# Kernel tuning notes

Measured on AMD Instinct MI355X. Metric: run time of the kernel, lower is better.

Reference implementation:

```python
import jax, jax.numpy as jnp
import numpy as np

B, L, C, S, W, R = 2, 16, 64, 64, 128, 32
MOD_HIDDEN = 32


def _conv3d(x, k, b, pad_hw):
    # x: (B,C,L,S,W), k: (O,I,1,kh,kw)
    y = jax.lax.conv_general_dilated(
        x, k, window_strides=(1, 1, 1),
        padding=((0, 0), (pad_hw, pad_hw), (pad_hw, pad_hw)),
        dimension_numbers=('NCDHW', 'OIDHW', 'NCDHW'))
    return y + b[None, :, None, None, None]


def setup_inputs() -> dict:
    key = jax.random.key(0)
    ks = jax.random.split(key, 16)
    d = {}
    d['x'] = jax.random.normal(ks[0], (B, L, C, S, W), jnp.float32)
    u1 = jax.random.uniform(ks[1], (C, R), jnp.float32)
    u2 = jax.random.uniform(ks[2], (C, R), jnp.float32)
    r_min, r_max = 0.8, 0.99
    d['nu_log'] = jnp.log(-0.5 * jnp.log(u1 * (r_max ** 2 - r_min ** 2) + r_min ** 2))
    d['theta_log'] = jnp.log(u2 * jnp.float32(2 * np.pi))
    d['disp_nu'] = jnp.zeros((C, R), jnp.float32)
    d['disp_theta'] = jnp.zeros((C, R), jnp.float32)
    d['mlp_w1'] = jax.random.normal(ks[3], (C, MOD_HIDDEN), jnp.float32) / np.sqrt(C).astype(np.float32)
    d['mlp_b1'] = jnp.zeros((MOD_HIDDEN,), jnp.float32)
    d['mlp_w2'] = jax.random.normal(ks[4], (MOD_HIDDEN, C * R * 2), jnp.float32) / np.sqrt(MOD_HIDDEN).astype(np.float32)
    d['mlp_b2'] = jnp.zeros((C * R * 2,), jnp.float32)
    d['forcing_scale'] = jnp.float32(0.1)
    d['U_row_r'] = jax.random.normal(ks[5], (C, S, R), jnp.float32) / np.sqrt(S).astype(np.float32)
    d['U_row_i'] = jax.random.normal(ks[6], (C, S, R), jnp.float32) / np.sqrt(S).astype(np.float32)
    d['V_col_r'] = jax.random.normal(ks[7], (C, W, R), jnp.float32) / np.sqrt(W).astype(np.float32)
    d['V_col_i'] = jax.random.normal(ks[8], (C, W, R), jnp.float32) / np.sqrt(W).astype(np.float32)
    d['proj_W_r'] = jax.random.normal(ks[9], (C, C), jnp.float32) / np.sqrt(C).astype(np.float32)
    d['proj_W_i'] = jax.random.normal(ks[10], (C, C), jnp.float32) / np.sqrt(C).astype(np.float32)
    d['proj_b_r'] = jnp.zeros((C,), jnp.float32)
    d['proj_b_i'] = jnp.zeros((C,), jnp.float32)
    fan = np.sqrt(C * 9).astype(np.float32)
    d['convr_k'] = jax.random.normal(ks[11], (C, C, 1, 3, 3), jnp.float32) / fan
    d['convr_b'] = jnp.zeros((C,), jnp.float32)
    d['convi_k'] = jax.random.normal(ks[12], (C, C, 1, 3, 3), jnp.float32) / fan
    d['convi_b'] = jnp.zeros((C,), jnp.float32)
    d['fuse_k'] = jax.random.normal(ks[13], (C, 2 * C, 1, 1, 1), jnp.float32) / np.sqrt(2 * C).astype(np.float32)
    d['fuse_b'] = jnp.zeros((C,), jnp.float32)
    d['ln_g'] = jnp.ones((S, W), jnp.float32)
    d['ln_b'] = jnp.zeros((S, W), jnp.float32)
    return d


def reference(x, nu_log, theta_log, disp_nu, disp_theta, mlp_w1, mlp_b1,
              mlp_w2, mlp_b2, forcing_scale, U_row_r, U_row_i, V_col_r,
              V_col_i, proj_W_r, proj_W_i, proj_b_r, proj_b_i, convr_k,
              convr_b, convi_k, convi_b, fuse_k, fuse_b, ln_g, ln_b):
    # Diagonal LRU poles lam = exp(-exp(nu) + i*exp(theta)), per (C,R)
    nu = jnp.exp(nu_log + disp_nu)
    theta = jnp.exp(theta_log + disp_theta)
    lam = jnp.exp(jax.lax.complex(-nu, theta))
    gamma = jnp.sqrt(jnp.clip(1.0 - jnp.abs(lam) ** 2, 1e-6, None))

    # Selective input-dependent forcing from spatially-pooled context
    ctx = x.mean(axis=(-2, -1))  # (B,L,C)
    f = jnp.tanh(ctx @ mlp_w1 + mlp_b1) @ mlp_w2 + mlp_b2
    f = f.reshape(ctx.shape[0], ctx.shape[1], C, R, 2)
    forcing = forcing_scale * jax.lax.complex(f[..., 0], f[..., 1])  # (B,L,C,R)

    # Low-rank complex spatial projection to rank-R state per channel
    U = jax.lax.complex(U_row_r, U_row_i)  # (C,S,R)
    V = jax.lax.complex(V_col_r, V_col_i)  # (C,W,R)
    xc = x.astype(jnp.complex64)
    u = jnp.einsum('blcsw,csr->blcwr', xc, jnp.conj(U))
    u = jnp.einsum('blcwr,cwr->blcr', u, jnp.conj(V))  # (B,L,C,R)
    u = gamma * u * (1.0 + forcing)

    # Diagonal linear recurrence h_t = lam*h_{t-1} + u_t via associative scan over L
    A = jnp.broadcast_to(lam[None, None], u.shape)

    def comb(e1, e2):
        a1, b1 = e1
        a2, b2 = e2
        return a1 * a2, a2 * b1 + b2

    _, h = jax.lax.associative_scan(comb, (A, u), axis=1)

    # Reconstruct spatial field from low-rank states
    t = jnp.einsum('blcr,csr->blcsr', h, U)
    y = jnp.einsum('blcsr,cwr->blcsw', t, V)  # (B,L,C,S,W) complex

    projW = jax.lax.complex(proj_W_r, proj_W_i)
    projb = jax.lax.complex(proj_b_r, proj_b_i)
    y = jnp.einsum('blcsw,oc->blosw', y, projW) + projb[None, None, :, None, None]

    # Post-recurrence spatial convs on real/imag parts, fuse, layernorm, residual
    yr = jnp.transpose(jnp.real(y), (0, 2, 1, 3, 4))  # (B,C,L,S,W)
    yi = jnp.transpose(jnp.imag(y), (0, 2, 1, 3, 4))
    yr = _conv3d(yr, convr_k, convr_b, 1)
    yi = _conv3d(yi, convi_k, convi_b, 1)
    fused = _conv3d(jnp.concatenate([yr, yi], axis=1), fuse_k, fuse_b, 0)
    fused = jnp.transpose(fused, (0, 2, 1, 3, 4))  # (B,L,C,S,W)

    mu = fused.mean(axis=(-2, -1), keepdims=True)
    var = fused.var(axis=(-2, -1), keepdims=True)
    normed = (fused - mu) / jnp.sqrt(var + 1e-5) * ln_g + ln_b
    return normed + x
```

## Files before the change

kernel.cpp:

```cpp
#include <hip/hip_runtime.h>

typedef unsigned short u16;
typedef unsigned int u32;
typedef __attribute__((ext_vector_type(8))) short short8;
typedef __attribute__((ext_vector_type(4))) float f32x4;
typedef __attribute__((ext_vector_type(16))) float f32x16;

constexpr int B = 2, L = 16, C = 64, S = 64, W = 128, R = 32, MH = 32;
constexpr int BL = B * L;
constexpr int SW = S * W;
constexpr int CR = C * R;
constexpr int F2 = C * R * 2;
constexpr int NVE = 64 * 4 * 4 * 64 * 8;
constexpr int NVD = 64 * 8 * 2 * 64 * 8;

constexpr int NB_PREP  = 8;
constexpr int NB_KEFF  = 289;
constexpr int NB_APACK = 64;
constexpr int NB_VPACK = (NVE + 2 * NVD + 255) / 256;
constexpr int NB_ALL   = NB_PREP + NB_KEFF + NB_APACK + NB_VPACK;

__device__ __forceinline__ float us2f(u16 h) { return __uint_as_float(((u32)h) << 16); }
__device__ __forceinline__ float bf_lo(u32 u) { return __uint_as_float(u << 16); }
__device__ __forceinline__ float bf_hi(u32 u) { return __uint_as_float(u & 0xffff0000u); }
__device__ __forceinline__ u16 f2bu(float f) {
  u32 u = __float_as_uint(f);
  u32 r = (u + 0x7fffu + ((u >> 16) & 1u)) >> 16;
  return (u16)r;
}
__device__ __forceinline__ u32 pack2(float lo, float hi) {
  return (u32)f2bu(lo) | ((u32)f2bu(hi) << 16);
}

__global__ void k_prep_all(
    const float* __restrict__ nu_log, const float* __restrict__ th_log,
    const float* __restrict__ dnu, const float* __restrict__ dth,
    float* __restrict__ lamr, float* __restrict__ lami, float* __restrict__ gam,
    const float* __restrict__ fuse_k, const float* __restrict__ fuse_b,
    const float* __restrict__ convr_k, const float* __restrict__ convr_b,
    const float* __restrict__ convi_k, const float* __restrict__ convi_b,
    u16* __restrict__ keff_bf, float* __restrict__ biaseff,
    const float* __restrict__ pWr, const float* __restrict__ pWi,
    u16* __restrict__ aproj,
    const float* __restrict__ Vr, const float* __restrict__ Vi,
    u16* __restrict__ venc, u16* __restrict__ vdecr, u16* __restrict__ vdeci) {
  int bid = blockIdx.x;
  int t = threadIdx.x;
  if (bid < NB_PREP) {
    int i = bid * 256 + t;
    if (i >= CR) return;
    float nu = expf(nu_log[i] + dnu[i]);
    float th = expf(th_log[i] + dth[i]);
    float mag = expf(-nu);
    lamr[i] = mag * cosf(th);
    lami[i] = mag * sinf(th);
    gam[i] = sqrtf(fmaxf(1.0f - mag * mag, 1e-6f));
  } else if (bid < NB_PREP + NB_KEFF) {
    int i = (bid - NB_PREP) * 256 + t;
    if (i < C * 2 * C * 9) {
      int o = i / (2 * C * 9);
      int rem = i - o * (2 * C * 9);
      int cin2 = rem / 9;
      int seg = rem - cin2 * 9;
      const float* ck = (cin2 < C) ? convr_k : convi_k;
      int cin = cin2 & (C - 1);
      int fbase = o * 2 * C + ((cin2 < C) ? 0 : C);
      float acc = 0.f;
      for (int m = 0; m < C; ++m)
        acc += fuse_k[fbase + m] * ck[(m * C + cin) * 9 + seg];
      int kslice = cin2 >> 4;
      int kk = cin2 & 15;
      int lane = (o & 31) | ((kk >> 3) << 5);
      int j = kk & 7;
      int m_tile = o >> 5;
      keff_bf[((((seg * 8 + kslice) * 2 + m_tile) * 64 + lane) << 3) + j] = f2bu(acc);
    } else if (i < C * 2 * C * 9 + C) {
      int o = i - C * 2 * C * 9;
      float acc = fuse_b[o];
      for (int m = 0; m < C; ++m) {
        acc += fuse_k[o * 2 * C + m] * convr_b[m];
        acc += fuse_k[o * 2 * C + C + m] * convi_b[m];
      }
      biaseff[o] = acc;
    }
  } else if (bid < NB_PREP + NB_KEFF + NB_APACK) {
    int i = (bid - NB_PREP - NB_KEFF) * 256 + t;
    if (i >= 128 * 128) return;
    int m = i >> 7, k = i & 127;
    int c = k >> 1, im = k & 1;
    int o = m & 63;
    float v;
    if (m < 64) v = im ? -pWi[o * 64 + c] : pWr[o * 64 + c];
    else        v = im ?  pWr[o * 64 + c] : pWi[o * 64 + c];
    aproj[i] = f2bu(v);
  } else {
    int i = (bid - NB_PREP - NB_KEFF - NB_APACK) * 256 + t;
    if (i < NVE) {
      int j = i & 7, lane = (i >> 3) & 63, ks = (i >> 9) & 3;
      int wv = (i >> 11) & 3, c = i >> 13;
      int n = wv * 16 + (lane & 15);
      int w = ks * 32 + ((lane >> 4) & 3) * 8 + j;
      float v = (n < 32) ? Vr[(size_t)c * 4096 + w * 32 + n]
                         : -Vi[(size_t)c * 4096 + w * 32 + (n - 32)];
      venc[i] = f2bu(v);
    } else if (i < NVE + 2 * NVD) {
      int ii = i - NVE;
      int isI = 0;
      if (ii >= NVD) { ii -= NVD; isI = 1; }
      int j = ii & 7, lane = (ii >> 3) & 63, ks = (ii >> 9) & 1;
      int g = (ii >> 10) & 7, c = ii >> 13;
      int w = g * 16 + (lane & 15);
      int k = ks * 32 + ((lane >> 4) & 3) * 8 + j;
      float v;
      if (!isI) v = (k < 32) ? Vr[(size_t)c * 4096 + w * 32 + k]
                             : -Vi[(size_t)c * 4096 + w * 32 + (k - 32)];
      else      v = (k < 32) ? Vi[(size_t)c * 4096 + w * 32 + k]
                             :  Vr[(size_t)c * 4096 + w * 32 + (k - 32)];
      (isI ? vdeci : vdecr)[ii] = f2bu(v);
    }
  }
}

__global__ __launch_bounds__(256) void k_mlp(
    const float* __restrict__ ctx, const float* __restrict__ w1, const float* __restrict__ b1,
    const float* __restrict__ w2, const float* __restrict__ b2, const float* __restrict__ fscale,
    float* __restrict__ forcing) {
  int bl = blockIdx.x >> 4;
  int kt = blockIdx.x & 15;
  int k0 = kt * 256;
  __shared__ float cv[C];
  __shared__ float hid[MH];
  __shared__ float lw2[MH * 256];
  int t = threadIdx.x;
  if (t < C) cv[t] = ctx[bl * C + t];
  for (int i = t; i < MH * 64; i += 256) {
    int j = i >> 6, q = i & 63;
    ((float4*)lw2)[i] = ((const float4*)(w2 + (size_t)j * F2 + k0))[q];
  }
  __syncthreads();
  if (t < MH) {
    float a = b1[t];
    for (int c2 = 0; c2 < C; ++c2) a += cv[c2] * w1[c2 * MH + t];
    hid[t] = tanhf(a);
  }
  __syncthreads();
  float scale = fscale[0];
  float a = b2[k0 + t];
#pragma unroll
  for (int j = 0; j < MH; ++j) a += hid[j] * lw2[j * 256 + t];
  forcing[(size_t)bl * F2 + k0 + t] = scale * a;
}

__global__ __launch_bounds__(256) void k_enc(
    const float* __restrict__ x, const u16* __restrict__ venc,
    const float* __restrict__ Ur, const float* __restrict__ Ui,
    float* __restrict__ ctx, float* __restrict__ u) {
  int blc = blockIdx.x;
  int c = blc & (C - 1);
  __shared__ __align__(16) char smem[35968];
  u16* xt = (u16*)smem;
  float* uldr = (float*)(smem + 17408);
  float* uldi = uldr + 2048;
  float* y1  = (float*)smem;
  float* part = (float*)(smem + 33792);
  float* red = (float*)(smem + 35840);
  int t = threadIdx.x;
  int lane = t & 63, wv = t >> 6;
  short8 bf[4];
  {
    const short8* vep = (const short8*)venc + ((size_t)(c * 4 + wv) * 4) * 64 + lane;
#pragma unroll
    for (int ks = 0; ks < 4; ++ks) bf[ks] = vep[ks * 64];
  }
  float sm = 0.f;
  {
    const float4* xp = (const float4*)(x + (size_t)blc * SW);
    for (int i = t; i < SW / 4; i += 256) {
      float4 v = xp[i];
      sm += v.x + v.y + v.z + v.w;
      int idx = i * 4, s = idx >> 7, w = idx & 127;
      u32* d = (u32*)&xt[s * 136 + w];
      d[0] = pack2(v.x, v.y);
      d[1] = pack2(v.z, v.w);
    }
  }
#pragma unroll
  for (int o = 32; o > 0; o >>= 1) sm += __shfl_down(sm, o, 64);
  if (lane == 0) red[wv] = sm;
  {
    const float4* urp = (const float4*)(Ur + (size_t)c * 2048);
    const float4* uip = (const float4*)(Ui + (size_t)c * 2048);
    float4* dr = (float4*)uldr;
    float4* di = (float4*)uldi;
    for (int i = t; i < 512; i += 256) { dr[i] = urp[i]; di[i] = uip[i]; }
  }
  __syncthreads();
  if (t == 0) ctx[blc] = (red[0] + red[1] + red[2] + red[3]) * (1.f / SW);
  int quad = lane >> 4, l15 = lane & 15;
  f32x4 zf = {0.f, 0.f, 0.f, 0.f};
  f32x4 acc[4] = {zf, zf, zf, zf};
#pragma unroll
  for (int ks = 0; ks < 4; ++ks) {
    int kofs = ks * 32 + quad * 8;
#pragma unroll
    for (int mt = 0; mt < 4; ++mt) {
      short8 af = *(const short8*)&xt[(mt * 16 + l15) * 136 + kofs];
      acc[mt] = __builtin_amdgcn_mfma_f32_16x16x32_bf16(af, bf[ks], acc[mt], 0, 0, 0);
    }
  }
  __syncthreads();
#pragma unroll
  for (int mt = 0; mt < 4; ++mt)
#pragma unroll
    for (int reg = 0; reg < 4; ++reg)
      y1[(mt * 16 + quad * 4 + reg) * 65 + wv * 16 + l15] = acc[mt][reg];
  __syncthreads();
  {
    int r = t & 31, sg = t >> 5;
    float pr = 0.f, pi = 0.f;
#pragma unroll
    for (int k = 0; k < 8; ++k) {
      int s = sg * 8 + k;
      float yr = y1[s * 65 + r], yi = y1[s * 65 + 32 + r];
      float ur = uldr[s * 32 + r], ui = uldi[s * 32 + r];
      pr += ur * yr + ui * yi;
      pi += ur * yi - ui * yr;
    }
    part[sg * 64 + r * 2]     = pr;
    part[sg * 64 + r * 2 + 1] = pi;
  }
  __syncthreads();
  if (t < 32) {
    float pr = 0.f, pi = 0.f;
#pragma unroll
    for (int sg = 0; sg < 8; ++sg) {
      pr += part[sg * 64 + t * 2];
      pi += part[sg * 64 + t * 2 + 1];
    }
    u[((size_t)blc * R + t) * 2]     = pr;
    u[((size_t)blc * R + t) * 2 + 1] = pi;
  }
}

__global__ __launch_bounds__(256) void k_scan(
    const float* __restrict__ lamr, const float* __restrict__ lami,
    const float* __restrict__ gam, const float* __restrict__ forcing,
    const float* __restrict__ u, float* __restrict__ h) {
  int b = blockIdx.x >> 4;
  int c0 = (blockIdx.x & 15) * 128;
  __shared__ float uld[L][256];
  __shared__ float fld[L][256];
  int t = threadIdx.x;
#pragma unroll
  for (int l = 0; l < L; ++l) {
    size_t base = ((size_t)(b * L + l) * CR + c0) * 2;
    uld[l][t] = u[base + t];
    fld[l][t] = forcing[base + t];
  }
  __syncthreads();
  if (t < 128) {
    int cr = c0 + t;
    float lr = lamr[cr], li = lami[cr], g = gam[cr];
    float hr = 0.f, hi = 0.f;
#pragma unroll
    for (int l = 0; l < L; ++l) {
      float ur0 = uld[l][t * 2], ui0 = uld[l][t * 2 + 1];
      float fr = fld[l][t * 2], fi = fld[l][t * 2 + 1];
      float ofr = 1.f + fr;
      float ur = g * (ur0 * ofr - ui0 * fi);
      float ui = g * (ur0 * fi + ui0 * ofr);
      float nr = lr * hr - li * hi + ur;
      float ni = lr * hi + li * hr + ui;
      hr = nr; hi = ni;
      uld[l][t * 2] = hr; uld[l][t * 2 + 1] = hi;
    }
  }
  __syncthreads();
#pragma unroll
  for (int l = 0; l < L; ++l) {
    size_t base = ((size_t)(b * L + l) * CR + c0) * 2;
    h[base + t] = uld[l][t];
  }
}

__global__ __launch_bounds__(256) void k_decode(
    const float* __restrict__ h,
    const float* __restrict__ Ur, const float* __restrict__ Ui,
    const u16* __restrict__ vdecr, const u16* __restrict__ vdeci,
    u32* __restrict__ y_cm32, int bl_base) {
  int bid = blockIdx.x;
  int c = bid & 63;
  int blh = bid >> 6;
  int bl = bl_base + blh;
  __shared__ __align__(16) u16 ldA[64 * 72];
  int t = threadIdx.x;
  {
    const float* hp = h + ((size_t)(bl * C + c) * R) * 2;
    const float* urp = Ur + (size_t)c * (S * R);
    const float* uip = Ui + (size_t)c * (S * R);
    for (int p = t; p < S * R; p += 256) {
      int s = p >> 5, r = p & 31;
      float hr = hp[r * 2], hi = hp[r * 2 + 1];
      float ur = urp[p], ui = uip[p];
      ldA[s * 72 + r]      = f2bu(hr * ur - hi * ui);
      ldA[s * 72 + 32 + r] = f2bu(hr * ui + hi * ur);
    }
  }
  __syncthreads();
  int lane = t & 63, q = t >> 6;
  int quad = lane >> 4, l15 = lane & 15;
  const short8* vdr = (const short8*)vdecr + (size_t)c * 16 * 64;
  const short8* vdi = (const short8*)vdeci + (size_t)c * 16 * 64;
  f32x4 zf = {0.f, 0.f, 0.f, 0.f};
  f32x4 accr[4][2], acci[4][2];
#pragma unroll
  for (int mt = 0; mt < 4; ++mt)
#pragma unroll
    for (int nt = 0; nt < 2; ++nt) { accr[mt][nt] = zf; acci[mt][nt] = zf; }
#pragma unroll
  for (int ks = 0; ks < 2; ++ks) {
    int kofs = ks * 32 + quad * 8;
    short8 af[4];
#pragma unroll
    for (int mt = 0; mt < 4; ++mt)
      af[mt] = *(const short8*)&ldA[(mt * 16 + l15) * 72 + kofs];
#pragma unroll
    for (int nt = 0; nt < 2; ++nt) {
      int g = q * 2 + nt;
      short8 br = vdr[(g * 2 + ks) * 64 + lane];
      short8 bi = vdi[(g * 2 + ks) * 64 + lane];
#pragma unroll
      for (int mt = 0; mt < 4; ++mt) {
        accr[mt][nt] = __builtin_amdgcn_mfma_f32_16x16x32_bf16(af[mt], br, accr[mt][nt], 0, 0, 0);
        acci[mt][nt] = __builtin_amdgcn_mfma_f32_16x16x32_bf16(af[mt], bi, acci[mt][nt], 0, 0, 0);
      }
    }
  }
  u32* dst = y_cm32 + ((size_t)(blh * 64 + c) << 13);
#pragma unroll
  for (int mt = 0; mt < 4; ++mt) {
#pragma unroll
    for (int nt = 0; nt < 2; ++nt) {
      int w = q * 32 + nt * 16 + l15;
#pragma unroll
      for (int reg = 0; reg < 4; ++reg) {
        int s = mt * 16 + quad * 4 + reg;
        dst[s * 128 + w] = pack2(accr[mt][nt][reg], acci[mt][nt][reg]);
      }
    }
  }
}

__global__ __launch_bounds__(256) void k_proj(
    const u32* __restrict__ y_cm32, const u16* __restrict__ aproj,
    const float* __restrict__ pbr, const float* __restrict__ pbi,
    u16* __restrict__ ynhwc, int bl_base) {
  int bid = blockIdx.x;
  int ntile = bid & 15;
  int blh = bid >> 4;
  int bl = bl_base + blh;
  __shared__ __align__(16) u16 lda[128 * 136];
  __shared__ __align__(16) u32 ldb[128 * 68];
  __shared__ float ldbias[128];
  int t = threadIdx.x;
  for (int i = t; i < 128 * 16; i += 256) {
    int m = i >> 4, qq = i & 15;
    ((uint4*)&lda[m * 136])[qq] = ((const uint4*)&aproj[m * 128])[qq];
  }
  if (t < 128) ldbias[t] = t < 64 ? pbr[t] : pbi[t - 64];

  int lane = t & 63, wv = t >> 6;
  int quad = lane >> 4, l15 = lane & 15;
  int cidx = t & 63, seg = t >> 6;
  f32x4 zf = {0.f, 0.f, 0.f, 0.f};

  for (int chunk = 0; chunk < 4; ++chunk) {
    int n0 = ntile * 512 + chunk * 128;
    __syncthreads();
    {
      const uint4* src = (const uint4*)(y_cm32 + (((size_t)(blh * 64 + cidx)) << 13) + n0 + seg * 32);
      u32 tmp[32];
#pragma unroll
      for (int qq = 0; qq < 8; ++qq) {
        uint4 v = src[qq];
        tmp[qq * 4] = v.x; tmp[qq * 4 + 1] = v.y; tmp[qq * 4 + 2] = v.z; tmp[qq * 4 + 3] = v.w;
      }
#pragma unroll
      for (int j = 0; j < 32; ++j)
        ldb[(seg * 32 + j) * 68 + cidx] = tmp[j];
    }
    __syncthreads();
    f32x4 acc[8][2];
#pragma unroll
    for (int mt = 0; mt < 8; ++mt) { acc[mt][0] = zf; acc[mt][1] = zf; }
    const u16* ldb16 = (const u16*)ldb;
#pragma unroll
    for (int ks = 0; ks < 4; ++ks) {
      int kofs = ks * 32 + quad * 8;
      short8 af[8];
#pragma unroll
      for (int mt = 0; mt < 8; ++mt)
        af[mt] = *(const short8*)&lda[(mt * 16 + l15) * 136 + kofs];
#pragma unroll
      for (int nt = 0; nt < 2; ++nt) {
        int nrow = wv * 32 + nt * 16 + l15;
        short8 bf = *(const short8*)&ldb16[nrow * 136 + kofs];
#pragma unroll
        for (int mt = 0; mt < 8; ++mt)
          acc[mt][nt] = __builtin_amdgcn_mfma_f32_16x16x32_bf16(af[mt], bf, acc[mt][nt], 0, 0, 0);
      }
    }
#pragma unroll
    for (int nt = 0; nt < 2; ++nt) {
      int n = n0 + wv * 32 + nt * 16 + l15;
      u16* drow = ynhwc + (((size_t)bl * SW + n) << 7);
#pragma unroll
      for (int mt = 0; mt < 8; ++mt) {
        int ch = mt * 16 + quad * 4;
        u32 lo = pack2(acc[mt][nt][0] + ldbias[ch],     acc[mt][nt][1] + ldbias[ch + 1]);
        u32 hi = pack2(acc[mt][nt][2] + ldbias[ch + 2], acc[mt][nt][3] + ldbias[ch + 3]);
        u32* dp = (u32*)(drow + ch);
        dp[0] = lo; dp[1] = hi;
      }
    }
  }
}

__global__ __launch_bounds__(256, 4) void k_conv(
    const u16* __restrict__ ynhwc, const u16* __restrict__ keff_bf,
    const float* __restrict__ biaseff, u16* __restrict__ fused) {
  int bid = blockIdx.x;
  int wt = bid & 1;
  int st = (bid >> 1) & 31;
  int bl = bid >> 6;
  int s0 = st * 2;
  int w0 = wt * 64;
  __shared__ __align__(16) u16 win[4][66][72];
  int t = threadIdx.x;
  int c_lo = (wt == 0) ? 1 : 0;
  int c_hi = (wt == 0) ? 66 : 65;
  uint4 z4 = make_uint4(0u, 0u, 0u, 0u);

  int lane = t & 63;
  int wv = t >> 6;
  int sr = wv & 1;
  int mt = wv >> 1;
  int l31 = lane & 31, khalf = lane >> 5;

  f32x16 acc0, acc1;
#pragma unroll
  for (int i = 0; i < 16; ++i) { acc0[i] = 0.f; acc1[i] = 0.f; }
  const short8* ap = (const short8*)keff_bf;
  short8 abuf[2];

#pragma unroll
  for (int p = 0; p < 2; ++p) {
    if (p) __syncthreads();
    for (int rr = 0; rr < 4; ++rr) {
      int rs = s0 - 1 + rr;
      if (rs < 0 || rs >= S) {
        for (int i = t; i < 66 * 8; i += 256) {
          int col = i >> 3, q = i & 7;
          ((uint4*)&win[rr][col][0])[q] = z4;
        }
      } else {
        if (wt == 0 && t < 8) ((uint4*)&win[rr][0][0])[t] = z4;
        if (wt == 1 && t < 8) ((uint4*)&win[rr][65][0])[t] = z4;
        const uint4* src = (const uint4*)(ynhwc +
            (((size_t)bl * S + rs) * W + (w0 - 1 + c_lo)) * 128 + p * 64);
        int n4 = (c_hi - c_lo) * 8;
        for (int i = t; i < n4; i += 256) {
          int col = i >> 3, q = i & 7;
          ((uint4*)&win[rr][c_lo + col][0])[q] = src[col * 16 + q];
        }
      }
    }
    __syncthreads();

    abuf[0] = ap[((p * 4) * 2 + mt) * 64 + lane];

#pragma unroll
    for (int m = 0; m < 36; ++m) {
      const int cur = m & 1;
      const int nxt = cur ^ 1;
      if (m < 35) {
        const int m1 = m + 1;
        abuf[nxt] = ap[((((m1 >> 2) * 8 + p * 4 + (m1 & 3)) * 2 + mt)) * 64 + lane];
      }
      const int seg = m >> 2;
      const int k4 = m & 3;
      const int dr = seg / 3;
      const int dc = seg - dr * 3;
      const u16* bb = &win[sr + dr][l31 + dc][k4 * 16 + khalf * 8];
      short8 b0 = *(const short8*)bb;
      short8 b1 = *(const short8*)(bb + 32 * 72);
      acc0 = __builtin_amdgcn_mfma_f32_32x32x16_bf16(abuf[cur], b0, acc0, 0, 0, 0);
      acc1 = __builtin_amdgcn_mfma_f32_32x32x16_bf16(abuf[cur], b1, acc1, 0, 0, 0);
    }
  }

  int s_out = s0 + sr;
#pragma unroll
  for (int reg = 0; reg < 16; ++reg) {
    int o = mt * 32 + (reg & 3) + 8 * (reg >> 2) + 4 * khalf;
    float bias = biaseff[o];
    size_t rowoff = ((size_t)(bl * C + o) * S + s_out) * W;
    fused[rowoff + w0 + l31]      = f2bu(acc0[reg] + bias);
    fused[rowoff + w0 + 32 + l31] = f2bu(acc1[reg] + bias);
  }
}

__global__ __launch_bounds__(256) void k_ln(
    const u16* __restrict__ fused,
    const float* __restrict__ ln_g, const float* __restrict__ ln_b,
    const float* __restrict__ x, float* __restrict__ out) {
  int blc = blockIdx.x;
  __shared__ u16 fs[SW];
  __shared__ float red[12];
  int t = threadIdx.x;
  const uint4* fp = (const uint4*)(fused + (size_t)blc * SW);
  float sm = 0.f, sq = 0.f;
  for (int i = t; i < SW / 8; i += 256) {
    uint4 v = fp[i];
    ((uint4*)fs)[i] = v;
    float f0 = bf_lo(v.x), f1 = bf_hi(v.x), f2 = bf_lo(v.y), f3 = bf_hi(v.y);
    float f4 = bf_lo(v.z), f5 = bf_hi(v.z), f6 = bf_lo(v.w), f7 = bf_hi(v.w);
    sm += f0 + f1 + f2 + f3 + f4 + f5 + f6 + f7;
    sq += f0 * f0 + f1 * f1 + f2 * f2 + f3 * f3 + f4 * f4 + f5 * f5 + f6 * f6 + f7 * f7;
  }
#pragma unroll
  for (int off = 32; off > 0; off >>= 1) {
    sm += __shfl_down(sm, off, 64);
    sq += __shfl_down(sq, off, 64);
  }
  int lane = t & 63, wid = t >> 6;
  if (lane == 0) { red[wid * 2] = sm; red[wid * 2 + 1] = sq; }
  __syncthreads();
  if (t == 0) {
    float S1 = red[0] + red[2] + red[4] + red[6];
    float S2 = red[1] + red[3] + red[5] + red[7];
    float mu = S1 * (1.f / SW);
    float var = S2 * (1.f / SW) - mu * mu;
    red[8] = mu;
    red[9] = rsqrtf(var + 1e-5f);
  }
  __syncthreads();
  float mu = red[8], rstd = red[9];
  const float4* xp4 = (const float4*)(x + (size_t)blc * SW);
  float4* op4 = (float4*)(out + (size_t)blc * SW);
  const float4* g4 = (const float4*)ln_g;
  const float4* b4 = (const float4*)ln_b;
  const uint2* fs2 = (const uint2*)fs;
  for (int i = t; i < SW / 4; i += 256) {
    uint2 fv = fs2[i];
    float4 xv = xp4[i];
    float4 gv = g4[i];
    float4 bv = b4[i];
    float4 o;
    o.x = (bf_lo(fv.x) - mu) * rstd * gv.x + bv.x + xv.x;
    o.y = (bf_hi(fv.x) - mu) * rstd * gv.y + bv.y + xv.y;
    o.z = (bf_lo(fv.y) - mu) * rstd * gv.z + bv.z + xv.z;
    o.w = (bf_hi(fv.y) - mu) * rstd * gv.w + bv.w + xv.w;
    op4[i] = o;
  }
}

extern "C" void kernel_launch(void* const* d_in, const int* in_sizes, int n_in,
                              void* d_out, int out_size, void* d_ws, size_t ws_size,
                              hipStream_t stream) {
  (void)in_sizes; (void)n_in; (void)out_size; (void)ws_size;
  const float* x       = (const float*)d_in[0];
  const float* nu_log  = (const float*)d_in[1];
  const float* th_log  = (const float*)d_in[2];
  const float* dnu     = (const float*)d_in[3];
  const float* dth     = (const float*)d_in[4];
  const float* w1      = (const float*)d_in[5];
  const float* b1      = (const float*)d_in[6];
  const float* w2      = (const float*)d_in[7];
  const float* b2      = (const float*)d_in[8];
  const float* fscale  = (const float*)d_in[9];
  const float* Ur      = (const float*)d_in[10];
  const float* Ui      = (const float*)d_in[11];
  const float* Vr      = (const float*)d_in[12];
  const float* Vi      = (const float*)d_in[13];
  const float* pWr     = (const float*)d_in[14];
  const float* pWi     = (const float*)d_in[15];
  const float* pbr     = (const float*)d_in[16];
  const float* pbi     = (const float*)d_in[17];
  const float* convr_k = (const float*)d_in[18];
  const float* convr_b = (const float*)d_in[19];
  const float* convi_k = (const float*)d_in[20];
  const float* convi_b = (const float*)d_in[21];
  const float* fuse_k  = (const float*)d_in[22];
  const float* fuse_b  = (const float*)d_in[23];
  const float* ln_g    = (const float*)d_in[24];
  const float* ln_b    = (const float*)d_in[25];
  float* out = (float*)d_out;

  char* ws = (char*)d_ws;
  float* lamr    = (float*)ws;
  float* lami    = lamr + 2048;
  float* gam     = lami + 2048;
  float* biaseff = gam + 2048;
  float* ctx     = biaseff + 64;
  float* forcing = ctx + 2048;
  float* ubuf    = forcing + 131072;
  float* hbuf    = ubuf + 131072;
  u16* keff_bf   = (u16*)(hbuf + 131072);
  u16* aproj     = keff_bf + 73728;
  u16* venc      = aproj + 16384;
  u16* vdecr     = venc + NVE;
  u16* vdeci     = vdecr + NVD;
  size_t off = ((size_t)((char*)(vdeci + NVD) - ws) + 255) & ~(size_t)255;
  u32* y_cm32    = (u32*)(ws + off);
  u16* fused     = (u16*)y_cm32;
  u16* ynhwc     = (u16*)(ws + off + (size_t)32 * 1024 * 1024);

  k_prep_all<<<NB_ALL, 256, 0, stream>>>(
      nu_log, th_log, dnu, dth, lamr, lami, gam,
      fuse_k, fuse_b, convr_k, convr_b, convi_k, convi_b, keff_bf, biaseff,
      pWr, pWi, aproj, Vr, Vi, venc, vdecr, vdeci);
  k_enc<<<BL * C, 256, 0, stream>>>(x, venc, Ur, Ui, ctx, ubuf);
  k_mlp<<<BL * 16, 256, 0, stream>>>(ctx, w1, b1, w2, b2, fscale, forcing);
  k_scan<<<32, 256, 0, stream>>>(lamr, lami, gam, forcing, ubuf, hbuf);
  k_decode<<<1024, 256, 0, stream>>>(hbuf, Ur, Ui, vdecr, vdeci, y_cm32, 0);
  k_proj<<<256, 256, 0, stream>>>(y_cm32, aproj, pbr, pbi, ynhwc, 0);
  k_decode<<<1024, 256, 0, stream>>>(hbuf, Ur, Ui, vdecr, vdeci, y_cm32, 16);
  k_proj<<<256, 256, 0, stream>>>(y_cm32, aproj, pbr, pbi, ynhwc, 16);
  k_conv<<<2048, 256, 0, stream>>>(ynhwc, keff_bf, biaseff, fused);
  k_ln<<<BL * C, 256, 0, stream>>>(fused, ln_g, ln_b, x, out);
}
```

Before: 332.5 us.

## Fuse modulation MLP and lambda prep into scan kernel; vectorize decode staging

The separate MLP kernel and the lambda/gamma prep blocks are removed. Each scan block now computes the hidden layer and forcing for its own channel chunk from shared memory, and derives lambda and gamma inline. This removes one kernel launch and the forcing round-trip through global memory. The cost is that the hidden-layer MLP is recomputed redundantly across the 16 chunk blocks, and the scan kernel uses more shared memory. Separately, the decode kernel's A-tile staging now uses float4 loads and 4-wide bf16 stores instead of scalar ones.

```diff
diff --git a/kernel.cpp b/kernel.cpp
--- a/kernel.cpp
+++ b/kernel.cpp
@@ -5,6 +5,7 @@
 typedef __attribute__((ext_vector_type(8))) short short8;
 typedef __attribute__((ext_vector_type(4))) float f32x4;
 typedef __attribute__((ext_vector_type(16))) float f32x16;
+typedef __attribute__((ext_vector_type(4))) unsigned short us4;
 
 constexpr int B = 2, L = 16, C = 64, S = 64, W = 128, R = 32, MH = 32;
 constexpr int BL = B * L;
@@ -14,11 +15,10 @@
 constexpr int NVE = 64 * 4 * 4 * 64 * 8;
 constexpr int NVD = 64 * 8 * 2 * 64 * 8;
 
-constexpr int NB_PREP  = 8;
 constexpr int NB_KEFF  = 289;
 constexpr int NB_APACK = 64;
 constexpr int NB_VPACK = (NVE + 2 * NVD + 255) / 256;
-constexpr int NB_ALL   = NB_PREP + NB_KEFF + NB_APACK + NB_VPACK;
+constexpr int NB_ALL   = NB_KEFF + NB_APACK + NB_VPACK;
 
 __device__ __forceinline__ float us2f(u16 h) { return __uint_as_float(((u32)h) << 16); }
 __device__ __forceinline__ float bf_lo(u32 u) { return __uint_as_float(u << 16); }
@@ -33,9 +33,6 @@
 }
 
 __global__ void k_prep_all(
-    const float* __restrict__ nu_log, const float* __restrict__ th_log,
-    const float* __restrict__ dnu, const float* __restrict__ dth,
-    float* __restrict__ lamr, float* __restrict__ lami, float* __restrict__ gam,
     const float* __restrict__ fuse_k, const float* __restrict__ fuse_b,
     const float* __restrict__ convr_k, const float* __restrict__ convr_b,
     const float* __restrict__ convi_k, const float* __restrict__ convi_b,
@@ -46,17 +43,8 @@
     u16* __restrict__ venc, u16* __restrict__ vdecr, u16* __restrict__ vdeci) {
   int bid = blockIdx.x;
   int t = threadIdx.x;
-  if (bid < NB_PREP) {
+  if (bid < NB_KEFF) {
     int i = bid * 256 + t;
-    if (i >= CR) return;
-    float nu = expf(nu_log[i] + dnu[i]);
-    float th = expf(th_log[i] + dth[i]);
-    float mag = expf(-nu);
-    lamr[i] = mag * cosf(th);
-    lami[i] = mag * sinf(th);
-    gam[i] = sqrtf(fmaxf(1.0f - mag * mag, 1e-6f));
-  } else if (bid < NB_PREP + NB_KEFF) {
-    int i = (bid - NB_PREP) * 256 + t;
     if (i < C * 2 * C * 9) {
       int o = i / (2 * C * 9);
       int rem = i - o * (2 * C * 9);
@@ -83,8 +71,8 @@
       }
       biaseff[o] = acc;
     }
-  } else if (bid < NB_PREP + NB_KEFF + NB_APACK) {
-    int i = (bid - NB_PREP - NB_KEFF) * 256 + t;
+  } else if (bid < NB_KEFF + NB_APACK) {
+    int i = (bid - NB_KEFF) * 256 + t;
     if (i >= 128 * 128) return;
     int m = i >> 7, k = i & 127;
     int c = k >> 1, im = k & 1;
@@ -94,7 +82,7 @@
     else        v = im ?  pWr[o * 64 + c] : pWi[o * 64 + c];
     aproj[i] = f2bu(v);
   } else {
-    int i = (bid - NB_PREP - NB_KEFF - NB_APACK) * 256 + t;
+    int i = (bid - NB_KEFF - NB_APACK) * 256 + t;
     if (i < NVE) {
       int j = i & 7, lane = (i >> 3) & 63, ks = (i >> 9) & 3;
       int wv = (i >> 11) & 3, c = i >> 13;
@@ -121,36 +109,6 @@
   }
 }
 
-__global__ __launch_bounds__(256) void k_mlp(
-    const float* __restrict__ ctx, const float* __restrict__ w1, const float* __restrict__ b1,
-    const float* __restrict__ w2, const float* __restrict__ b2, const float* __restrict__ fscale,
-    float* __restrict__ forcing) {
-  int bl = blockIdx.x >> 4;
-  int kt = blockIdx.x & 15;
-  int k0 = kt * 256;
-  __shared__ float cv[C];
-  __shared__ float hid[MH];
-  __shared__ float lw2[MH * 256];
-  int t = threadIdx.x;
-  if (t < C) cv[t] = ctx[bl * C + t];
-  for (int i = t; i < MH * 64; i += 256) {
-    int j = i >> 6, q = i & 63;
-    ((float4*)lw2)[i] = ((const float4*)(w2 + (size_t)j * F2 + k0))[q];
-  }
-  __syncthreads();
-  if (t < MH) {
-    float a = b1[t];
-    for (int c2 = 0; c2 < C; ++c2) a += cv[c2] * w1[c2 * MH + t];
-    hid[t] = tanhf(a);
-  }
-  __syncthreads();
-  float scale = fscale[0];
-  float a = b2[k0 + t];
-#pragma unroll
-  for (int j = 0; j < MH; ++j) a += hid[j] * lw2[j * 256 + t];
-  forcing[(size_t)bl * F2 + k0 + t] = scale * a;
-}
-
 __global__ __launch_bounds__(256) void k_enc(
     const float* __restrict__ x, const u16* __restrict__ venc,
     const float* __restrict__ Ur, const float* __restrict__ Ui,
@@ -243,24 +201,61 @@
 }
 
 __global__ __launch_bounds__(256) void k_scan(
-    const float* __restrict__ lamr, const float* __restrict__ lami,
-    const float* __restrict__ gam, const float* __restrict__ forcing,
+    const float* __restrict__ nu_log, const float* __restrict__ th_log,
+    const float* __restrict__ dnu, const float* __restrict__ dth,
+    const float* __restrict__ ctx, const float* __restrict__ w1,
+    const float* __restrict__ b1, const float* __restrict__ w2,
+    const float* __restrict__ b2, const float* __restrict__ fscale,
     const float* __restrict__ u, float* __restrict__ h) {
   int b = blockIdx.x >> 4;
-  int c0 = (blockIdx.x & 15) * 128;
+  int chunk = blockIdx.x & 15;
+  int c0 = chunk * 128;
+  int k0 = c0 * 2;
   __shared__ float uld[L][256];
   __shared__ float fld[L][256];
+  __shared__ float w2t[MH][256];
+  __shared__ float ctxv[16][64];
+  __shared__ float hid[16][MH];
   int t = threadIdx.x;
 #pragma unroll
   for (int l = 0; l < L; ++l) {
     size_t base = ((size_t)(b * L + l) * CR + c0) * 2;
     uld[l][t] = u[base + t];
-    fld[l][t] = forcing[base + t];
+  }
+  for (int i = t; i < MH * 64; i += 256) {
+    int j = i >> 6, q = i & 63;
+    ((float4*)&w2t[j][0])[q] = ((const float4*)(w2 + (size_t)j * F2 + k0))[q];
+  }
+  ((float4*)&ctxv[0][0])[t] = ((const float4*)(ctx + (size_t)b * L * C))[t];
+  __syncthreads();
+  for (int job = t; job < 16 * MH; job += 256) {
+    int l = job >> 5, m = job & 31;
+    float a = b1[m];
+#pragma unroll
+    for (int c2 = 0; c2 < C; ++c2) a += ctxv[l][c2] * w1[c2 * MH + m];
+    hid[l][m] = tanhf(a);
+  }
+  __syncthreads();
+  {
+    float scale = fscale[0];
+    float bb = b2[k0 + t];
+#pragma unroll
+    for (int l = 0; l < L; ++l) {
+      float a = bb;
+#pragma unroll
+      for (int j = 0; j < MH; ++j) a += hid[l][j] * w2t[j][t];
+      fld[l][t] = scale * a;
+    }
   }
   __syncthreads();
   if (t < 128) {
     int cr = c0 + t;
-    float lr = lamr[cr], li = lami[cr], g = gam[cr];
+    float nu = expf(nu_log[cr] + dnu[cr]);
+    float th = expf(th_log[cr] + dth[cr]);
+    float mag = expf(-nu);
+    float lr = mag * cosf(th);
+    float li = mag * sinf(th);
+    float g = sqrtf(fmaxf(1.0f - mag * mag, 1e-6f));
     float hr = 0.f, hi = 0.f;
 #pragma unroll
     for (int l = 0; l < L; ++l) {
@@ -298,12 +293,19 @@
     const float* hp = h + ((size_t)(bl * C + c) * R) * 2;
     const float* urp = Ur + (size_t)c * (S * R);
     const float* uip = Ui + (size_t)c * (S * R);
-    for (int p = t; p < S * R; p += 256) {
-      int s = p >> 5, r = p & 31;
-      float hr = hp[r * 2], hi = hp[r * 2 + 1];
-      float ur = urp[p], ui = uip[p];
-      ldA[s * 72 + r]      = f2bu(hr * ur - hi * ui);
-      ldA[s * 72 + 32 + r] = f2bu(hr * ui + hi * ur);
+    for (int i = t; i < 512; i += 256) {
+      int s = i >> 3, r0 = (i & 7) * 4;
+      float4 ur = *(const float4*)(urp + s * 32 + r0);
+      float4 ui = *(const float4*)(uip + s * 32 + r0);
+      float4 h0 = *(const float4*)(hp + r0 * 2);
+      float4 h1 = *(const float4*)(hp + r0 * 2 + 4);
+      us4 re, im;
+      re.x = f2bu(h0.x * ur.x - h0.y * ui.x); im.x = f2bu(h0.x * ui.x + h0.y * ur.x);
+      re.y = f2bu(h0.z * ur.y - h0.w * ui.y); im.y = f2bu(h0.z * ui.y + h0.w * ur.y);
+      re.z = f2bu(h1.x * ur.z - h1.y * ui.z); im.z = f2bu(h1.x * ui.z + h1.y * ur.z);
+      re.w = f2bu(h1.z * ur.w - h1.w * ui.w); im.w = f2bu(h1.z * ui.w + h1.w * ur.w);
+      *(us4*)&ldA[s * 72 + r0]      = re;
+      *(us4*)&ldA[s * 72 + 32 + r0] = im;
     }
   }
   __syncthreads();
@@ -615,14 +617,14 @@
   u32* y_cm32    = (u32*)(ws + off);
   u16* fused     = (u16*)y_cm32;
   u16* ynhwc     = (u16*)(ws + off + (size_t)32 * 1024 * 1024);
+  (void)lamr; (void)lami; (void)gam; (void)forcing;
 
   k_prep_all<<<NB_ALL, 256, 0, stream>>>(
-      nu_log, th_log, dnu, dth, lamr, lami, gam,
       fuse_k, fuse_b, convr_k, convr_b, convi_k, convi_b, keff_bf, biaseff,
       pWr, pWi, aproj, Vr, Vi, venc, vdecr, vdeci);
   k_enc<<<BL * C, 256, 0, stream>>>(x, venc, Ur, Ui, ctx, ubuf);
-  k_mlp<<<BL * 16, 256, 0, stream>>>(ctx, w1, b1, w2, b2, fscale, forcing);
-  k_scan<<<32, 256, 0, stream>>>(lamr, lami, gam, forcing, ubuf, hbuf);
+  k_scan<<<32, 256, 0, stream>>>(nu_log, th_log, dnu, dth, ctx, w1, b1, w2, b2,
+                                 fscale, ubuf, hbuf);
   k_decode<<<1024, 256, 0, stream>>>(hbuf, Ur, Ui, vdecr, vdeci, y_cm32, 0);
   k_proj<<<256, 256, 0, stream>>>(y_cm32, aproj, pbr, pbi, ynhwc, 0);
   k_decode<<<1024, 256, 0, stream>>>(hbuf, Ur, Ui, vdecr, vdeci, y_cm32, 16);
```

Measured after the change: 330.4 us. No clear change (-0.6%).
